# Kernel tuning notes

Measured on AMD Instinct MI355X. Metric: run time of the kernel, lower is better.

Reference implementation:

```python
import jax, jax.numpy as jnp
import numpy as np
from jax import lax

B, C, H, W = 4, 64, 128, 128
G, K, RED = 16, 7, 4        # groups, kernel size, reduce ratio
CR = C // RED               # reduced channels for kernel generation
EPS = 1e-5                  # BatchNorm eps (torch default)
DN = ('NCHW', 'OIHW', 'NCHW')


def setup_inputs() -> dict:
    key = jax.random.key(0)
    ks = jax.random.split(key, 5)
    return {
        'input': jax.random.normal(ks[0], (B, C, H, W), jnp.float32),
        # initial_mapping: depthwise 3x3 conv + pointwise 1x1 conv (bias=False)
        'w_dw': jax.random.normal(ks[1], (C, 1, 3, 3), jnp.float32) * 0.1,
        'w_pw': jax.random.normal(ks[2], (C, C), jnp.float32) * (1.0 / np.sqrt(C)),
        # sigma_mapping BatchNorm affine params
        'bn_gamma': jnp.ones((CR,), jnp.float32),
        'bn_beta': jnp.zeros((CR,), jnp.float32),
        # reduce / span 1x1 convs (bias=False)
        'w_reduce': jax.random.normal(ks[3], (CR, C), jnp.float32) * (1.0 / np.sqrt(C)),
        'w_span': jax.random.normal(ks[4], (K * K * G, CR), jnp.float32) * (1.0 / np.sqrt(CR)),
    }


def reference(input, w_dw, w_pw, bn_gamma, bn_beta, w_reduce, w_span):
    x = input
    # initial mapping: depthwise 3x3 (pad 1) then 1x1 pointwise
    h = lax.conv_general_dilated(x, w_dw, (1, 1), [(1, 1), (1, 1)],
                                 feature_group_count=C, dimension_numbers=DN)
    h = jnp.einsum('bchw,oc->bohw', h, w_pw)
    # unfold -> [B, C*K*K, H, W] with channel-major feature ordering (matches torch Unfold)
    patches = lax.conv_general_dilated_patches(h, (K, K), (1, 1), [(3, 3), (3, 3)],
                                               dimension_numbers=DN)
    patches = patches.reshape(B, G, C // G, K * K, H, W)
    # kernel generation: o_mapping is identity (stride 1 avg pool), then reduce -> BN(train) -> ReLU -> span
    r = jnp.einsum('bchw,oc->bohw', x, w_reduce)           # [B, CR, H, W]
    mean = r.mean(axis=(0, 2, 3), keepdims=True)
    var = r.var(axis=(0, 2, 3), keepdims=True)             # biased var, as torch BN training
    r = (r - mean) * lax.rsqrt(var + EPS) * bn_gamma[None, :, None, None] + bn_beta[None, :, None, None]
    r = jax.nn.relu(r)
    kern = jnp.einsum('bchw,oc->bohw', r, w_span)          # [B, G*K*K, H, W]
    kern = kern.reshape(B, G, 1, K * K, H, W)
    out = (kern * patches).sum(axis=3)                     # [B, G, C//G, H, W]
    return out.reshape(B, C, H, W)
```

## Files before the change

### kernel.cpp

```cpp
#include <hip/hip_runtime.h>

typedef _Float16 half2v __attribute__((ext_vector_type(2)));
typedef _Float16 half4v __attribute__((ext_vector_type(4)));
typedef _Float16 half8v __attribute__((ext_vector_type(8)));
typedef float f32x4 __attribute__((ext_vector_type(4)));

__global__ void k_prep(const float* __restrict__ wspan, _Float16* __restrict__ w16,
                       float* __restrict__ stats){
  int i = blockIdx.x * 256 + threadIdx.x;
  if (i < 32) stats[i] = 0.f;
  if (i < 12544) w16[i] = (_Float16)wspan[i];
}

__launch_bounds__(256, 4)
__global__ void k_front(const float* __restrict__ in, const float* __restrict__ wdw,
                        const float* __restrict__ wpw, const float* __restrict__ wred,
                        float* __restrict__ h, float* __restrict__ r,
                        float* __restrict__ stats){
  __shared__ float4 s_in4[4][10][12];
  __shared__ __attribute__((aligned(16))) _Float16 s_dwh[64][72];
  __shared__ __attribute__((aligned(16))) _Float16 s_cvh[64][72];
  __shared__ float s_red[4][32];
  int t = threadIdx.x;
  int w = t >> 6, lane = t & 63;
  int lx = lane & 7, ly = lane >> 3;
  int c15 = lane & 15, hi = lane >> 4;
  int blk = blockIdx.x;
  blk = ((blk & 7) << 7) | (blk >> 3);
  int tile = blk & 255, b = blk >> 8;
  int x0 = (tile & 15) << 3, y0 = (tile >> 4) << 3;
  const float* inb = in + ((long)b << 20) + ((long)(w << 2) << 14);

  const float* ap = wpw + (((w << 4) + c15) << 6) + (hi << 3);
  float4 ap0 = *(const float4*)(ap);
  float4 ap1 = *(const float4*)(ap + 4);
  float4 ap2 = *(const float4*)(ap + 32);
  float4 ap3 = *(const float4*)(ap + 36);
  const float* arp = wred + (c15 << 6) + (hi << 3);
  float4 ar0 = *(const float4*)(arp);
  float4 ar1 = *(const float4*)(arp + 4);
  float4 ar2 = *(const float4*)(arp + 32);
  float4 ar3 = *(const float4*)(arp + 36);
  half8v a_pw0 = {(_Float16)ap0.x,(_Float16)ap0.y,(_Float16)ap0.z,(_Float16)ap0.w,
                  (_Float16)ap1.x,(_Float16)ap1.y,(_Float16)ap1.z,(_Float16)ap1.w};
  half8v a_pw1 = {(_Float16)ap2.x,(_Float16)ap2.y,(_Float16)ap2.z,(_Float16)ap2.w,
                  (_Float16)ap3.x,(_Float16)ap3.y,(_Float16)ap3.z,(_Float16)ap3.w};
  half8v a_rd0 = {(_Float16)ar0.x,(_Float16)ar0.y,(_Float16)ar0.z,(_Float16)ar0.w,
                  (_Float16)ar1.x,(_Float16)ar1.y,(_Float16)ar1.z,(_Float16)ar1.w};
  half8v a_rd1 = {(_Float16)ar2.x,(_Float16)ar2.y,(_Float16)ar2.z,(_Float16)ar2.w,
                  (_Float16)ar3.x,(_Float16)ar3.y,(_Float16)ar3.z,(_Float16)ar3.w};

  int p0 = lane, p1 = lane + 64;
  int ry0 = p0 / 10, rx0 = p0 - ry0 * 10;
  int ry1 = p1 / 10, rx1 = p1 - ry1 * 10;
  int yy0 = y0 + ry0 - 1, xx0 = x0 + rx0 - 1;
  int yy1 = y0 + ry1 - 1, xx1 = x0 + rx1 - 1;
  bool ok0 = (unsigned)yy0 < 128u && (unsigned)xx0 < 128u;
  bool ok1 = (p1 < 100) && ((unsigned)yy1 < 128u) && ((unsigned)xx1 < 128u);
  int o0 = (yy0 << 7) + xx0, o1 = (yy1 << 7) + xx1;

  float4 v0 = make_float4(0.f, 0.f, 0.f, 0.f), v1 = make_float4(0.f, 0.f, 0.f, 0.f);
  if (ok0){ v0.x = inb[o0]; v0.y = inb[o0 + 16384]; v0.z = inb[o0 + 32768]; v0.w = inb[o0 + 49152]; }
  if (ok1){ v1.x = inb[o1]; v1.y = inb[o1 + 16384]; v1.z = inb[o1 + 32768]; v1.w = inb[o1 + 49152]; }

  for (int q = 0; q < 4; q++){
    s_in4[w][ry0][rx0] = v0;
    if (p1 < 100) s_in4[w][ry1][rx1] = v1;
    __builtin_amdgcn_wave_barrier();

    if (q < 3){
      const float* pq = inb + ((long)(q + 1) << 18);
      v0 = make_float4(0.f, 0.f, 0.f, 0.f); v1 = make_float4(0.f, 0.f, 0.f, 0.f);
      if (ok0){ v0.x = pq[o0]; v0.y = pq[o0 + 16384]; v0.z = pq[o0 + 32768]; v0.w = pq[o0 + 49152]; }
      if (ok1){ v1.x = pq[o1]; v1.y = pq[o1 + 16384]; v1.z = pq[o1 + 32768]; v1.w = pq[o1 + 49152]; }
    }

    int wdbase = __builtin_amdgcn_readfirstlane(((q << 4) + (w << 2)) * 9);
    const float* wd = wdw + wdbase;
    float4 a = make_float4(0.f, 0.f, 0.f, 0.f);
    float4 cv = make_float4(0.f, 0.f, 0.f, 0.f);
    #pragma unroll
    for (int dy = 0; dy < 3; dy++){
      #pragma unroll
      for (int dx = 0; dx < 3; dx++){
        float4 v = s_in4[w][ly + dy][lx + dx];
        int k = dy * 3 + dx;
        a.x += v.x * wd[k];
        a.y += v.y * wd[9 + k];
        a.z += v.z * wd[18 + k];
        a.w += v.w * wd[27 + k];
        if (k == 4) cv = v;
      }
    }

    int cb = (q << 4) + (w << 2);
    half4v ah = {(_Float16)a.x, (_Float16)a.y, (_Float16)a.z, (_Float16)a.w};
    half4v eh = {(_Float16)cv.x, (_Float16)cv.y, (_Float16)cv.z, (_Float16)cv.w};
    *(half4v*)&s_dwh[lane][cb] = ah;
    *(half4v*)&s_cvh[lane][cb] = eh;
  }

  __syncthreads();

  f32x4 z = {0.f, 0.f, 0.f, 0.f};
  f32x4 acc[4] = {z, z, z, z};
  #pragma unroll
  for (int tt = 0; tt < 4; tt++){
    half8v b0 = *(const half8v*)&s_dwh[(tt << 4) + c15][hi << 3];
    half8v b1 = *(const half8v*)&s_dwh[(tt << 4) + c15][32 + (hi << 3)];
    acc[tt] = __builtin_amdgcn_mfma_f32_16x16x32_f16(a_pw0, b0, acc[tt], 0, 0, 0);
    acc[tt] = __builtin_amdgcn_mfma_f32_16x16x32_f16(a_pw1, b1, acc[tt], 0, 0, 0);
  }
  #pragma unroll
  for (int tt = 0; tt < 4; tt++){
    int px = (tt << 4) + c15, py = px >> 3, pxl = px & 7;
    long base = ((long)((b << 6) + (w << 4) + (hi << 2)) << 14) + ((y0 + py) << 7) + x0 + pxl;
    #pragma unroll
    for (int rr = 0; rr < 4; rr++) h[base + ((long)rr << 14)] = acc[tt][rr];
  }

  f32x4 rac = z;
  {
    half8v b0 = *(const half8v*)&s_cvh[(w << 4) + c15][hi << 3];
    half8v b1 = *(const half8v*)&s_cvh[(w << 4) + c15][32 + (hi << 3)];
    rac = __builtin_amdgcn_mfma_f32_16x16x32_f16(a_rd0, b0, rac, 0, 0, 0);
    rac = __builtin_amdgcn_mfma_f32_16x16x32_f16(a_rd1, b1, rac, 0, 0, 0);
  }
  {
    int px = (w << 4) + c15, py = px >> 3, pxl = px & 7;
    long rbase = ((long)b << 18) + ((long)(hi << 2) << 14) + ((y0 + py) << 7) + x0 + pxl;
    #pragma unroll
    for (int rr = 0; rr < 4; rr++) r[rbase + ((long)rr << 14)] = rac[rr];
  }

  #pragma unroll
  for (int rr = 0; rr < 4; rr++){
    float v = rac[rr], s2 = v * v;
    #pragma unroll
    for (int m = 1; m < 16; m <<= 1){
      v  += __shfl_xor(v,  m, 64);
      s2 += __shfl_xor(s2, m, 64);
    }
    if (c15 == 0){
      int ch = (hi << 2) + rr;
      s_red[w][2 * ch]     = v;
      s_red[w][2 * ch + 1] = s2;
    }
  }
  __syncthreads();
  if (t < 32){
    float sum = s_red[0][t] + s_red[1][t] + s_red[2][t] + s_red[3][t];
    atomicAdd(&stats[t], sum);
  }
}

__launch_bounds__(256)
__global__ void k_main(const float* __restrict__ h, const float* __restrict__ r,
                       const float* __restrict__ stats, const float* __restrict__ gamma,
                       const float* __restrict__ beta, const _Float16* __restrict__ w16,
                       float* __restrict__ out){
  __shared__ float4 s_h4[22][24];
  __shared__ float  s_sb[32];
  int t = threadIdx.x;
  int g = blockIdx.y, b = blockIdx.z;
  int bx = blockIdx.x;
  bx = ((bx & 7) << 3) | (bx >> 3);
  int tx0 = (bx & 7) << 4, ty0 = (bx >> 3) << 4;

  int ltx = t & 15, lty = t >> 4;
  int px = tx0 + ltx, py = ty0 + lty;
  const float* rp = r + ((long)b << 18) + (py << 7) + px;
  float rraw[16];
  #pragma unroll
  for (int c = 0; c < 16; c++) rraw[c] = rp[(long)c << 14];

  const float* hp = h + (((long)(b * 64 + g * 4)) << 14);
  for (int p = t; p < 484; p += 256){
    int ry = p / 22, rx = p - ry * 22;
    int yy = ty0 + ry - 3, xx = tx0 + rx - 3;
    float4 v = make_float4(0.f, 0.f, 0.f, 0.f);
    if ((unsigned)yy < 128u && (unsigned)xx < 128u){
      int o = (yy << 7) + xx;
      v.x = hp[o];
      v.y = hp[o + 16384];
      v.z = hp[o + 32768];
      v.w = hp[o + 49152];
    }
    s_h4[ry][rx] = v;
  }

  if (t < 16){
    const float inv_n = 1.52587890625e-5f;
    float mean = stats[2 * t] * inv_n;
    float var  = stats[2 * t + 1] * inv_n - mean * mean;
    float inv  = rsqrtf(var + 1e-5f);
    float sc   = gamma[t] * inv;
    s_sb[2 * t]     = sc;
    s_sb[2 * t + 1] = beta[t] - mean * sc;
  }
  __syncthreads();

  float rv[16];
  #pragma unroll
  for (int c = 0; c < 16; c++)
    rv[c] = fmaxf(rraw[c] * s_sb[2 * c] + s_sb[2 * c + 1], 0.f);
#if __has_builtin(__builtin_amdgcn_fdot2)
  half2v rv2[8];
  #pragma unroll
  for (int j = 0; j < 8; j++){
    half2v pk; pk[0] = (_Float16)rv[2 * j]; pk[1] = (_Float16)rv[2 * j + 1];
    rv2[j] = pk;
  }
#endif

  const _Float16* wg = w16 + g * 784;
#if __has_builtin(__builtin_amdgcn_fdot2)
  const half2v* wg2 = (const half2v*)wg;
#endif
  float acc0 = 0.f, acc1 = 0.f, acc2 = 0.f, acc3 = 0.f;
  #pragma unroll
  for (int kh = 0; kh < 7; kh++){
    #pragma unroll
    for (int kw = 0; kw < 7; kw++){
      int k = kh * 7 + kw;
      float kv = 0.f;
#if __has_builtin(__builtin_amdgcn_fdot2)
      #pragma unroll
      for (int j = 0; j < 8; j++)
        kv = __builtin_amdgcn_fdot2(rv2[j], wg2[k * 8 + j], kv, false);
#else
      #pragma unroll
      for (int c = 0; c < 16; c++) kv += rv[c] * (float)wg[k * 16 + c];
#endif
      float4 hv = s_h4[lty + kh][ltx + kw];
      acc0 += kv * hv.x;
      acc1 += kv * hv.y;
      acc2 += kv * hv.z;
      acc3 += kv * hv.w;
    }
  }

  long obase = (((long)(b * 64 + g * 4)) << 14) + (py << 7) + px;
  out[obase]         = acc0;
  out[obase + 16384] = acc1;
  out[obase + 32768] = acc2;
  out[obase + 49152] = acc3;
}

extern "C" void kernel_launch(void* const* d_in, const int* in_sizes, int n_in,
                              void* d_out, int out_size, void* d_ws, size_t ws_size,
                              hipStream_t stream){
  const float* in       = (const float*)d_in[0];
  const float* w_dw     = (const float*)d_in[1];
  const float* w_pw     = (const float*)d_in[2];
  const float* gamma    = (const float*)d_in[3];
  const float* beta     = (const float*)d_in[4];
  const float* w_reduce = (const float*)d_in[5];
  const float* w_span   = (const float*)d_in[6];
  float* out = (float*)d_out;

  float* ws    = (float*)d_ws;
  float* h     = ws;
  float* r     = ws + 4194304;
  float* stats = ws + 5242880;
  _Float16* w16 = (_Float16*)(ws + 5242944);

  k_prep <<<49, 256, 0, stream>>>(w_span, w16, stats);
  k_front<<<1024, 256, 0, stream>>>(in, w_dw, w_pw, w_reduce, h, r, stats);
  dim3 grid(64, 16, 4);
  k_main <<<grid, 256, 0, stream>>>(h, r, stats, gamma, beta, w16, out);
}
```

Baseline: 126.2 us.

## Store intermediates as fp16 in group-interleaved layout and fold weight prep into front kernel

The h and r intermediates are now written as fp16 and interleaved per group and pixel, so k_main loads each pixel's 4 group channels with one half4 load and all 16 r channels with two half8 loads. This halves intermediate memory traffic and makes the gathers vectorized. The separate k_prep launch is removed: the w_span conversion moves into k_front and the stats zeroing becomes a memset. The kernel-weight dot product is also split into two accumulator chains. The cost is extra fp16 rounding on h and r, which adds precision error.

```diff
diff --git a/kernel.cpp b/kernel.cpp
--- a/kernel.cpp
+++ b/kernel.cpp
@@ -5,18 +5,12 @@
 typedef _Float16 half8v __attribute__((ext_vector_type(8)));
 typedef float f32x4 __attribute__((ext_vector_type(4)));
 
-__global__ void k_prep(const float* __restrict__ wspan, _Float16* __restrict__ w16,
-                       float* __restrict__ stats){
-  int i = blockIdx.x * 256 + threadIdx.x;
-  if (i < 32) stats[i] = 0.f;
-  if (i < 12544) w16[i] = (_Float16)wspan[i];
-}
-
 __launch_bounds__(256, 4)
 __global__ void k_front(const float* __restrict__ in, const float* __restrict__ wdw,
                         const float* __restrict__ wpw, const float* __restrict__ wred,
-                        float* __restrict__ h, float* __restrict__ r,
-                        float* __restrict__ stats){
+                        const float* __restrict__ wspan,
+                        _Float16* __restrict__ h16, _Float16* __restrict__ r16,
+                        float* __restrict__ stats, _Float16* __restrict__ w16){
   __shared__ float4 s_in4[4][10][12];
   __shared__ __attribute__((aligned(16))) _Float16 s_dwh[64][72];
   __shared__ __attribute__((aligned(16))) _Float16 s_cvh[64][72];
@@ -25,8 +19,14 @@
   int w = t >> 6, lane = t & 63;
   int lx = lane & 7, ly = lane >> 3;
   int c15 = lane & 15, hi = lane >> 4;
-  int blk = blockIdx.x;
-  blk = ((blk & 7) << 7) | (blk >> 3);
+  int blk0 = blockIdx.x;
+
+  {
+    int i = blk0 * 256 + t;
+    if (i < 12544) w16[i] = (_Float16)wspan[i];
+  }
+
+  int blk = ((blk0 & 7) << 7) | (blk0 >> 3);
   int tile = blk & 255, b = blk >> 8;
   int x0 = (tile & 15) << 3, y0 = (tile >> 4) << 3;
   const float* inb = in + ((long)b << 20) + ((long)(w << 2) << 14);
@@ -50,18 +50,18 @@
   half8v a_rd1 = {(_Float16)ar2.x,(_Float16)ar2.y,(_Float16)ar2.z,(_Float16)ar2.w,
                   (_Float16)ar3.x,(_Float16)ar3.y,(_Float16)ar3.z,(_Float16)ar3.w};
 
-  int p0 = lane, p1 = lane + 64;
-  int ry0 = p0 / 10, rx0 = p0 - ry0 * 10;
-  int ry1 = p1 / 10, rx1 = p1 - ry1 * 10;
+  int p1 = lane + 64;
+  int ry0 = lane / 10, rx0 = lane - ry0 * 10;
+  int ry1 = p1 / 10,   rx1 = p1 - ry1 * 10;
   int yy0 = y0 + ry0 - 1, xx0 = x0 + rx0 - 1;
   int yy1 = y0 + ry1 - 1, xx1 = x0 + rx1 - 1;
   bool ok0 = (unsigned)yy0 < 128u && (unsigned)xx0 < 128u;
   bool ok1 = (p1 < 100) && ((unsigned)yy1 < 128u) && ((unsigned)xx1 < 128u);
   int o0 = (yy0 << 7) + xx0, o1 = (yy1 << 7) + xx1;
 
-  float4 v0 = make_float4(0.f, 0.f, 0.f, 0.f), v1 = make_float4(0.f, 0.f, 0.f, 0.f);
-  if (ok0){ v0.x = inb[o0]; v0.y = inb[o0 + 16384]; v0.z = inb[o0 + 32768]; v0.w = inb[o0 + 49152]; }
-  if (ok1){ v1.x = inb[o1]; v1.y = inb[o1 + 16384]; v1.z = inb[o1 + 32768]; v1.w = inb[o1 + 49152]; }
+  float4 v0 = make_float4(0.f,0.f,0.f,0.f), v1 = make_float4(0.f,0.f,0.f,0.f);
+  if (ok0){ v0.x = inb[o0]; v0.y = inb[o0+16384]; v0.z = inb[o0+32768]; v0.w = inb[o0+49152]; }
+  if (ok1){ v1.x = inb[o1]; v1.y = inb[o1+16384]; v1.z = inb[o1+32768]; v1.w = inb[o1+49152]; }
 
   for (int q = 0; q < 4; q++){
     s_in4[w][ry0][rx0] = v0;
@@ -70,15 +70,15 @@
 
     if (q < 3){
       const float* pq = inb + ((long)(q + 1) << 18);
-      v0 = make_float4(0.f, 0.f, 0.f, 0.f); v1 = make_float4(0.f, 0.f, 0.f, 0.f);
-      if (ok0){ v0.x = pq[o0]; v0.y = pq[o0 + 16384]; v0.z = pq[o0 + 32768]; v0.w = pq[o0 + 49152]; }
-      if (ok1){ v1.x = pq[o1]; v1.y = pq[o1 + 16384]; v1.z = pq[o1 + 32768]; v1.w = pq[o1 + 49152]; }
+      v0 = make_float4(0.f,0.f,0.f,0.f); v1 = make_float4(0.f,0.f,0.f,0.f);
+      if (ok0){ v0.x = pq[o0]; v0.y = pq[o0+16384]; v0.z = pq[o0+32768]; v0.w = pq[o0+49152]; }
+      if (ok1){ v1.x = pq[o1]; v1.y = pq[o1+16384]; v1.z = pq[o1+32768]; v1.w = pq[o1+49152]; }
     }
 
     int wdbase = __builtin_amdgcn_readfirstlane(((q << 4) + (w << 2)) * 9);
     const float* wd = wdw + wdbase;
-    float4 a = make_float4(0.f, 0.f, 0.f, 0.f);
-    float4 cv = make_float4(0.f, 0.f, 0.f, 0.f);
+    float4 a = make_float4(0.f,0.f,0.f,0.f);
+    float4 cv = make_float4(0.f,0.f,0.f,0.f);
     #pragma unroll
     for (int dy = 0; dy < 3; dy++){
       #pragma unroll
@@ -92,17 +92,16 @@
         if (k == 4) cv = v;
       }
     }
-
     int cb = (q << 4) + (w << 2);
-    half4v ah = {(_Float16)a.x, (_Float16)a.y, (_Float16)a.z, (_Float16)a.w};
-    half4v eh = {(_Float16)cv.x, (_Float16)cv.y, (_Float16)cv.z, (_Float16)cv.w};
+    half4v ah = {(_Float16)a.x,(_Float16)a.y,(_Float16)a.z,(_Float16)a.w};
+    half4v eh = {(_Float16)cv.x,(_Float16)cv.y,(_Float16)cv.z,(_Float16)cv.w};
     *(half4v*)&s_dwh[lane][cb] = ah;
     *(half4v*)&s_cvh[lane][cb] = eh;
   }
 
   __syncthreads();
 
-  f32x4 z = {0.f, 0.f, 0.f, 0.f};
+  f32x4 z = {0.f,0.f,0.f,0.f};
   f32x4 acc[4] = {z, z, z, z};
   #pragma unroll
   for (int tt = 0; tt < 4; tt++){
@@ -113,10 +112,13 @@
   }
   #pragma unroll
   for (int tt = 0; tt < 4; tt++){
-    int px = (tt << 4) + c15, py = px >> 3, pxl = px & 7;
-    long base = ((long)((b << 6) + (w << 4) + (hi << 2)) << 14) + ((y0 + py) << 7) + x0 + pxl;
-    #pragma unroll
-    for (int rr = 0; rr < 4; rr++) h[base + ((long)rr << 14)] = acc[tt][rr];
+    int px = (tt << 4) + c15;
+    int pyl = px >> 3, pxl = px & 7;
+    int gout = (w << 2) + hi;
+    long off = ((((long)((b << 4) + gout)) << 14) + ((y0 + pyl) << 7) + x0 + pxl) << 2;
+    half4v hv = {(_Float16)acc[tt][0], (_Float16)acc[tt][1],
+                 (_Float16)acc[tt][2], (_Float16)acc[tt][3]};
+    *(half4v*)&h16[off] = hv;
   }
 
   f32x4 rac = z;
@@ -127,10 +129,11 @@
     rac = __builtin_amdgcn_mfma_f32_16x16x32_f16(a_rd1, b1, rac, 0, 0, 0);
   }
   {
-    int px = (w << 4) + c15, py = px >> 3, pxl = px & 7;
-    long rbase = ((long)b << 18) + ((long)(hi << 2) << 14) + ((y0 + py) << 7) + x0 + pxl;
-    #pragma unroll
-    for (int rr = 0; rr < 4; rr++) r[rbase + ((long)rr << 14)] = rac[rr];
+    int px = (w << 4) + c15;
+    int pyl = px >> 3, pxl = px & 7;
+    long roff = ((((long)b << 14) + ((y0 + pyl) << 7) + x0 + pxl) << 4) + (hi << 2);
+    half4v rv4 = {(_Float16)rac[0], (_Float16)rac[1], (_Float16)rac[2], (_Float16)rac[3]};
+    *(half4v*)&r16[roff] = rv4;
   }
 
   #pragma unroll
@@ -155,7 +158,7 @@
 }
 
 __launch_bounds__(256)
-__global__ void k_main(const float* __restrict__ h, const float* __restrict__ r,
+__global__ void k_main(const _Float16* __restrict__ h16, const _Float16* __restrict__ r16,
                        const float* __restrict__ stats, const float* __restrict__ gamma,
                        const float* __restrict__ beta, const _Float16* __restrict__ w16,
                        float* __restrict__ out){
@@ -169,22 +172,19 @@
 
   int ltx = t & 15, lty = t >> 4;
   int px = tx0 + ltx, py = ty0 + lty;
-  const float* rp = r + ((long)b << 18) + (py << 7) + px;
-  float rraw[16];
-  #pragma unroll
-  for (int c = 0; c < 16; c++) rraw[c] = rp[(long)c << 14];
-
-  const float* hp = h + (((long)(b * 64 + g * 4)) << 14);
+
+  const _Float16* rp = r16 + ((((long)b << 14) + (py << 7) + px) << 4);
+  half8v ra = *(const half8v*)rp;
+  half8v rb = *(const half8v*)(rp + 8);
+
+  const _Float16* hp = h16 + (((long)((b << 4) + g)) << 16);
   for (int p = t; p < 484; p += 256){
     int ry = p / 22, rx = p - ry * 22;
     int yy = ty0 + ry - 3, xx = tx0 + rx - 3;
-    float4 v = make_float4(0.f, 0.f, 0.f, 0.f);
+    float4 v = make_float4(0.f,0.f,0.f,0.f);
     if ((unsigned)yy < 128u && (unsigned)xx < 128u){
-      int o = (yy << 7) + xx;
-      v.x = hp[o];
-      v.y = hp[o + 16384];
-      v.z = hp[o + 32768];
-      v.w = hp[o + 49152];
+      half4v hh = *(const half4v*)&hp[(long)(((yy << 7) + xx) << 2)];
+      v = make_float4((float)hh[0], (float)hh[1], (float)hh[2], (float)hh[3]);
     }
     s_h4[ry][rx] = v;
   }
@@ -202,13 +202,15 @@
 
   float rv[16];
   #pragma unroll
-  for (int c = 0; c < 16; c++)
-    rv[c] = fmaxf(rraw[c] * s_sb[2 * c] + s_sb[2 * c + 1], 0.f);
+  for (int c = 0; c < 8; c++){
+    rv[c]     = fmaxf((float)ra[c] * s_sb[2*c]     + s_sb[2*c+1],     0.f);
+    rv[c + 8] = fmaxf((float)rb[c] * s_sb[2*(c+8)] + s_sb[2*(c+8)+1], 0.f);
+  }
 #if __has_builtin(__builtin_amdgcn_fdot2)
   half2v rv2[8];
   #pragma unroll
   for (int j = 0; j < 8; j++){
-    half2v pk; pk[0] = (_Float16)rv[2 * j]; pk[1] = (_Float16)rv[2 * j + 1];
+    half2v pk; pk[0] = (_Float16)rv[2*j]; pk[1] = (_Float16)rv[2*j+1];
     rv2[j] = pk;
   }
 #endif
@@ -223,15 +225,21 @@
     #pragma unroll
     for (int kw = 0; kw < 7; kw++){
       int k = kh * 7 + kw;
-      float kv = 0.f;
+      float kv0 = 0.f, kv1 = 0.f;
 #if __has_builtin(__builtin_amdgcn_fdot2)
       #pragma unroll
-      for (int j = 0; j < 8; j++)
-        kv = __builtin_amdgcn_fdot2(rv2[j], wg2[k * 8 + j], kv, false);
+      for (int j = 0; j < 4; j++){
+        kv0 = __builtin_amdgcn_fdot2(rv2[j],     wg2[k*8 + j],     kv0, false);
+        kv1 = __builtin_amdgcn_fdot2(rv2[j + 4], wg2[k*8 + j + 4], kv1, false);
+      }
 #else
       #pragma unroll
-      for (int c = 0; c < 16; c++) kv += rv[c] * (float)wg[k * 16 + c];
+      for (int c = 0; c < 8; c++){
+        kv0 += rv[c]     * (float)wg[k*16 + c];
+        kv1 += rv[c + 8] * (float)wg[k*16 + c + 8];
+      }
 #endif
+      float kv = kv0 + kv1;
       float4 hv = s_h4[lty + kh][ltx + kw];
       acc0 += kv * hv.x;
       acc1 += kv * hv.y;
@@ -240,7 +248,7 @@
     }
   }
 
-  long obase = (((long)(b * 64 + g * 4)) << 14) + (py << 7) + px;
+  long obase = (((long)((b << 6) + (g << 2))) << 14) + (py << 7) + px;
   out[obase]         = acc0;
   out[obase + 16384] = acc1;
   out[obase + 32768] = acc2;
@@ -259,14 +267,14 @@
   const float* w_span   = (const float*)d_in[6];
   float* out = (float*)d_out;
 
-  float* ws    = (float*)d_ws;
-  float* h     = ws;
-  float* r     = ws + 4194304;
-  float* stats = ws + 5242880;
-  _Float16* w16 = (_Float16*)(ws + 5242944);
-
-  k_prep <<<49, 256, 0, stream>>>(w_span, w16, stats);
-  k_front<<<1024, 256, 0, stream>>>(in, w_dw, w_pw, w_reduce, h, r, stats);
+  _Float16* h16 = (_Float16*)d_ws;
+  _Float16* r16 = h16 + 4194304;
+  _Float16* w16 = r16 + 1048576;
+  float* stats  = (float*)(w16 + 12544);
+
+  hipMemsetAsync(stats, 0, 32 * sizeof(float), stream);
+  k_front<<<1024, 256, 0, stream>>>(in, w_dw, w_pw, w_reduce, w_span,
+                                    h16, r16, stats, w16);
   dim3 grid(64, 16, 4);
-  k_main <<<grid, 256, 0, stream>>>(h, r, stats, gamma, beta, w16, out);
+  k_main <<<grid, 256, 0, stream>>>(h16, r16, stats, gamma, beta, w16, out);
 }
```

Measured after the change: 125.1 us. Within noise of the previous version (-0.9%).
